# Optimization experiments

Hardware: AMD Instinct MI355X
Metric: run time of the kernel (lower is better)

The kernel has to match this reference:

```python
import jax, jax.numpy as jnp
import numpy as np

N = 100_000          # nodes
E_RAND = 1_600_000   # random edges (avg degree 16)
IN, H, F, SEQ = 64, 4, 16, 10
FLAT = H * F * SEQ   # 640, MLP input width
MLP_DIMS = [FLAT, 180, 150, 128, 80, 64, 32, 1]


def setup_inputs() -> dict:
    key = jax.random.key(0)
    ks = jax.random.split(key, 32)
    x = jax.random.normal(ks[0], (N, IN), jnp.float32)
    # edges + self loops (dgl.add_self_loop)
    src = jnp.concatenate([jax.random.randint(ks[1], (E_RAND,), 0, N), jnp.arange(N)]).astype(jnp.int32)
    dst = jnp.concatenate([jax.random.randint(ks[2], (E_RAND,), 0, N), jnp.arange(N)]).astype(jnp.int32)
    inp = {"x": x, "src": src, "dst": dst}
    # GATConv params (fc has no bias in DGL; bias added post-aggregation)
    inp["fc_w"] = (jax.random.normal(ks[3], (IN, H * F), jnp.float32) / np.sqrt(IN).astype(np.float32))
    inp["bias"] = jnp.zeros((H * F,), jnp.float32)
    inp["attn_l"] = jax.random.normal(ks[4], (H, F), jnp.float32) * 0.1
    inp["attn_r"] = jax.random.normal(ks[5], (H, F), jnp.float32) * 0.1
    # deep MLP params
    for i in range(7):
        di, do = MLP_DIMS[i], MLP_DIMS[i + 1]
        inp[f"w{i+1}"] = jax.random.normal(ks[6 + i], (di, do), jnp.float32) / np.sqrt(di).astype(np.float32)
        inp[f"b{i+1}"] = jnp.zeros((do,), jnp.float32)
    inp["wt"] = jax.random.normal(ks[20], (FLAT, 1), jnp.float32) / np.sqrt(FLAT).astype(np.float32)
    return inp


def reference(x, src, dst, fc_w, bias, attn_l, attn_r,
              w1, b1, w2, b2, w3, b3, w4, b4, w5, b5, w6, b6, w7, b7, wt):
    # --- GATConv ---
    feat = (x @ fc_w).reshape(N, H, F)                      # [N,H,F]
    el = jnp.einsum('nhf,hf->nh', feat, attn_l)             # [N,H]
    er = jnp.einsum('nhf,hf->nh', feat, attn_r)
    e = jax.nn.leaky_relu(el[src] + er[dst], 0.2)           # [E,H]
    # edge softmax over incoming edges of each dst node
    m = jax.ops.segment_max(e, dst, num_segments=N)         # [N,H]
    ez = jnp.exp(e - m[dst])
    denom = jax.ops.segment_sum(ez, dst, num_segments=N)
    alpha = ez / denom[dst]                                 # [E,H]
    msg = alpha[:, :, None] * feat[src]                     # [E,H,F]
    out = jax.ops.segment_sum(msg, dst, num_segments=N) + bias.reshape(1, H, F)
    # --- flatten SEQ nodes per path, deep MLP + linear_trans ---
    g = out.reshape(N // SEQ, FLAT)                         # [P,640]
    h = g
    layers = [(w1, b1), (w2, b2), (w3, b3), (w4, b4), (w5, b5), (w6, b6), (w7, b7)]
    for i, (w, b) in enumerate(layers):
        h = h @ w + b
        if i < len(layers) - 1:
            h = jax.nn.relu(h)
    wx = g @ wt                                             # [P,1]
    return h + wx
```

## Files before the change

kernel.cpp:

```cpp
#include <hip/hip_runtime.h>
#include <hip/hip_bf16.h>
#include <hip/hip_fp16.h>

#define N_NODES 100000
#define P_PATHS 10000
#define NBUK 391
#define FEAT_BLKS 782
#define HIST_BLKS 416
#define WPREP_BLKS 94
#define LOG2E 1.4426950408889634f
#define BC_CAP 5120

typedef __attribute__((ext_vector_type(8))) short s16x8;
typedef __attribute__((ext_vector_type(4))) short s16x4;
typedef __attribute__((ext_vector_type(4))) float f32x4;
typedef __attribute__((ext_vector_type(8))) _Float16 f16x8;
typedef __attribute__((ext_vector_type(2))) _Float16 f16x2;

__device__ __forceinline__ short f2bf(float v) {
    return __builtin_bit_cast(short, __float2bfloat16(v));
}
__device__ __forceinline__ float bf2f(short s) {
    return __bfloat162float(__builtin_bit_cast(__hip_bfloat16, s));
}
__device__ __forceinline__ float h2f(short s) {
    return __half2float(__builtin_bit_cast(__half, s));
}
__device__ __forceinline__ short f2h(float v) {
    return __builtin_bit_cast(short, __float2half(v));
}

__global__ __launch_bounds__(256) void k_fused1(const float* __restrict__ x,
                                                const float* __restrict__ fc_w,
                                                const float* __restrict__ attn_l,
                                                const float* __restrict__ attn_r,
                                                __half* __restrict__ feat,
                                                float* __restrict__ el,
                                                float* __restrict__ er,
                                                const int* __restrict__ dst,
                                                int* __restrict__ buktot,
                                                const float* __restrict__ w1,
                                                const float* __restrict__ w2,
                                                const float* __restrict__ w3,
                                                const float* __restrict__ w4,
                                                const float* __restrict__ w5,
                                                const float* __restrict__ w6,
                                                short* __restrict__ wf, int E) {
    __shared__ float s_w[64 * 64];
    __shared__ float s_wx[64 * 16];
    __shared__ int hcnt[NBUK];
    int tid = threadIdx.x;
    int bb = blockIdx.x;

    if (bb < FEAT_BLKS) {
        for (int i = tid; i < 4096; i += 256) s_w[i] = fc_w[i];
        __syncthreads();
        for (int i = tid; i < 1024; i += 256) {
            int k = i >> 4, c = i & 15;
            float v = 0.f;
            if (c < 8) {
                int h = c & 3;
                const float* av = (c < 4) ? attn_l : attn_r;
                for (int f = 0; f < 16; ++f) v += s_w[k * 64 + h * 16 + f] * av[h * 16 + f];
            }
            s_wx[i] = v * LOG2E;
        }
        __syncthreads();

        int w = tid >> 6, l = tid & 63;
        int c_lane = l & 15, kg = l >> 4;

        s16x8 wh[5][2], wlo[5][2];
#pragma unroll
        for (int ct = 0; ct < 5; ++ct)
#pragma unroll
            for (int ks = 0; ks < 2; ++ks) {
                s16x8 h8, l8;
#pragma unroll
                for (int i = 0; i < 8; ++i) {
                    int k = ks * 32 + kg * 8 + i;
                    float v = (ct < 4) ? s_w[k * 64 + ct * 16 + c_lane]
                                       : s_wx[k * 16 + c_lane];
                    short hi = f2bf(v);
                    h8[i] = hi;
                    l8[i] = f2bf(v - bf2f(hi));
                }
                wh[ct][ks] = h8;
                wlo[ct][ks] = l8;
            }

        int nbase = bb * 128 + w * 32;
#pragma unroll 1
        for (int mt = 0; mt < 2; ++mt) {
            int m0 = nbase + mt * 16;
            if (m0 >= N_NODES) break;
            int arow = m0 + c_lane;
            size_t axoff = (size_t)(arow < N_NODES ? arow : N_NODES - 1) * 64;
            s16x8 ah[2], alo[2];
#pragma unroll
            for (int ks = 0; ks < 2; ++ks) {
                const float* xp = x + axoff + ks * 32 + kg * 8;
                float4 v0 = *(const float4*)xp;
                float4 v1 = *(const float4*)(xp + 4);
                float vv[8] = {v0.x, v0.y, v0.z, v0.w, v1.x, v1.y, v1.z, v1.w};
                s16x8 h8, l8;
#pragma unroll
                for (int i = 0; i < 8; ++i) {
                    short hi = f2bf(vv[i]);
                    h8[i] = hi;
                    l8[i] = f2bf(vv[i] - bf2f(hi));
                }
                ah[ks] = h8;
                alo[ks] = l8;
            }
            int r0 = m0 + kg * 4;
#pragma unroll
            for (int ct = 0; ct < 5; ++ct) {
                f32x4 acc = {0.f, 0.f, 0.f, 0.f};
#pragma unroll
                for (int ks = 0; ks < 2; ++ks) {
                    acc = __builtin_amdgcn_mfma_f32_16x16x32_bf16(ah[ks], wh[ct][ks], acc, 0, 0, 0);
                    acc = __builtin_amdgcn_mfma_f32_16x16x32_bf16(ah[ks], wlo[ct][ks], acc, 0, 0, 0);
                    acc = __builtin_amdgcn_mfma_f32_16x16x32_bf16(alo[ks], wh[ct][ks], acc, 0, 0, 0);
                }
                if (ct < 4) {
#pragma unroll
                    for (int j = 0; j < 4; ++j) {
                        int r = r0 + j;
                        if (r < N_NODES)
                            feat[(size_t)r * 64 + ct * 16 + c_lane] = __float2half(acc[j]);
                    }
                } else {
                    if (c_lane < 4) {
#pragma unroll
                        for (int j = 0; j < 4; ++j) {
                            int r = r0 + j;
                            if (r < N_NODES) el[r * 4 + c_lane] = acc[j];
                        }
                    } else if (c_lane < 8) {
#pragma unroll
                        for (int j = 0; j < 4; ++j) {
                            int r = r0 + j;
                            if (r < N_NODES) er[r * 4 + (c_lane - 4)] = acc[j];
                        }
                    }
                }
            }
        }
    } else if (bb < FEAT_BLKS + HIST_BLKS) {
        int hb = bb - FEAT_BLKS;
        for (int i = tid; i < NBUK; i += 256) hcnt[i] = 0;
        __syncthreads();
#pragma unroll
        for (int j = 0; j < 4; ++j) {
            int i = hb * 4096 + j * 1024 + tid * 4;
            if (i + 3 < E) {
                int4 d4 = *(const int4*)(dst + i);
                atomicAdd(&hcnt[d4.x >> 8], 1);
                atomicAdd(&hcnt[d4.y >> 8], 1);
                atomicAdd(&hcnt[d4.z >> 8], 1);
                atomicAdd(&hcnt[d4.w >> 8], 1);
            } else {
                for (int k = i; k < E && k < i + 4; ++k)
                    atomicAdd(&hcnt[dst[k] >> 8], 1);
            }
        }
        __syncthreads();
        for (int i = tid; i < NBUK; i += 256)
            if (hcnt[i]) atomicAdd(buktot + i, hcnt[i]);
    } else {
        const int nblk[6] = {240, 60, 40, 20, 12, 4};
        const int din_[6] = {640, 180, 150, 128, 80, 64};
        const int dout_[6] = {180, 150, 128, 80, 64, 32};
        const int ks_[6]  = {20, 6, 5, 4, 3, 2};
        const int off_[6] = {0, 122880, 153600, 174080, 184320, 190464};
        const float* wp[6] = {w1, w2, w3, w4, w5, w6};

        int b = (bb - FEAT_BLKS - HIST_BLKS) * 4 + (tid >> 6);
        int layer = 0;
        while (layer < 5 && b >= nblk[layer]) { b -= nblk[layer]; ++layer; }
        int KS = ks_[layer];
        int ct = b / KS, ks = b % KS;
        int l = tid & 63;
        int c = ct * 16 + (l & 15);
        int k0 = ks * 32 + ((l >> 4) * 8);
        int din = din_[layer], dout = dout_[layer];
        const float* w = wp[layer];
        s16x8 vh;
#pragma unroll
        for (int i = 0; i < 8; ++i) {
            int k = k0 + i;
            float v = (k < din && c < dout) ? w[k * dout + c] : 0.f;
            vh[i] = f2h(v);
        }
        size_t o = (size_t)off_[layer] + ((size_t)(ct * KS + ks) * 64 + l) * 8;
        *(s16x8*)(wf + o) = vh;
    }
}

__global__ __launch_bounds__(512) void k_scanB(const int* __restrict__ buktot,
                                               int* __restrict__ bukstart,
                                               int* __restrict__ bukptr,
                                               int* __restrict__ rowptr, int E) {
    __shared__ int s[512];
    int tid = threadIdx.x;
    int v = (tid < NBUK) ? buktot[tid] : 0;
    s[tid] = v;
    __syncthreads();
    for (int off = 1; off < 512; off <<= 1) {
        int t = (tid >= off) ? s[tid - off] : 0;
        __syncthreads();
        s[tid] += t;
        __syncthreads();
    }
    int excl = s[tid] - v;
    if (tid < NBUK) { bukstart[tid] = excl; bukptr[tid] = excl; }
    if (tid == 0) { bukstart[NBUK] = E; rowptr[N_NODES] = E; }
}

__global__ __launch_bounds__(256) void k_bucketA(const int* __restrict__ src,
                                                 const int* __restrict__ dst,
                                                 int* __restrict__ bukptr,
                                                 unsigned* __restrict__ pair, int E) {
    __shared__ int cnt[NBUK];
    __shared__ int seg[NBUK];
    __shared__ int gbase[NBUK];
    __shared__ unsigned sbuf[2048];
    __shared__ int gaddr[2048];
    __shared__ int csum[256];
    int tid = threadIdx.x;
    for (int i = tid; i < NBUK; i += 256) cnt[i] = 0;
    __syncthreads();
    int b0 = blockIdx.x * 2048;
    int sv[8], dv[8], off[8];
#pragma unroll
    for (int j = 0; j < 8; ++j) {
        int i = b0 + j * 256 + tid;
        if (i < E) {
            sv[j] = src[i];
            dv[j] = dst[i];
            off[j] = atomicAdd(&cnt[dv[j] >> 8], 1);
        } else {
            dv[j] = -1; sv[j] = 0; off[j] = 0;
        }
    }
    __syncthreads();
    int c0 = (2 * tid < NBUK) ? cnt[2 * tid] : 0;
    int c1 = (2 * tid + 1 < NBUK) ? cnt[2 * tid + 1] : 0;
    int psum = c0 + c1;
    csum[tid] = psum;
    __syncthreads();
    for (int o2 = 1; o2 < 256; o2 <<= 1) {
        int t = (tid >= o2) ? csum[tid - o2] : 0;
        __syncthreads();
        csum[tid] += t;
        __syncthreads();
    }
    int pexcl = csum[tid] - psum;
    if (2 * tid < NBUK) seg[2 * tid] = pexcl;
    if (2 * tid + 1 < NBUK) seg[2 * tid + 1] = pexcl + c0;
    __syncthreads();
    for (int i = tid; i < NBUK; i += 256)
        gbase[i] = cnt[i] ? atomicAdd(bukptr + i, cnt[i]) : 0;
    __syncthreads();
#pragma unroll
    for (int j = 0; j < 8; ++j) {
        if (dv[j] >= 0) {
            int b = dv[j] >> 8;
            int k = seg[b] + off[j];
            sbuf[k] = (unsigned)sv[j] | ((unsigned)(dv[j] & 255) << 17);
            gaddr[k] = gbase[b] + off[j];
        }
    }
    __syncthreads();
    int tot = E - b0; if (tot > 2048) tot = 2048;
    for (int k = tid; k < tot; k += 256)
        pair[gaddr[k]] = sbuf[k];
}

__global__ __launch_bounds__(256) void k_bucketC(const unsigned* __restrict__ pair,
                                                 const int* __restrict__ bukstart,
                                                 int* __restrict__ rowptr,
                                                 int* __restrict__ csr, int E) {
    __shared__ int cnt[256];
    __shared__ int s[256];
    __shared__ int wofs[256];
    __shared__ unsigned sp[BC_CAP];
    int buk = blockIdx.x, tid = threadIdx.x;
    int p0 = bukstart[buk], p1 = bukstart[buk + 1];
    int len = p1 - p0;
    bool fits = (len <= BC_CAP);
    cnt[tid] = 0;
    __syncthreads();
    for (int i = p0 + tid; i < p1; i += 256) {
        unsigned v = pair[i];
        if (fits) sp[i - p0] = v;
        atomicAdd(&cnt[v >> 17], 1);
    }
    __syncthreads();
    int v = cnt[tid];
    s[tid] = v;
    __syncthreads();
    for (int off = 1; off < 256; off <<= 1) {
        int t = (tid >= off) ? s[tid - off] : 0;
        __syncthreads();
        s[tid] += t;
        __syncthreads();
    }
    int r = p0 + s[tid] - v;
    wofs[tid] = r;
    int node = (buk << 8) + tid;
    if (node < N_NODES) rowptr[node] = r;
    __syncthreads();
    for (int i = p0 + tid; i < p1; i += 256) {
        unsigned p = fits ? sp[i - p0] : pair[i];
        int pos = atomicAdd(&wofs[p >> 17], 1);
        csr[pos] = (int)(p & 0x1FFFFu);
    }
}

__global__ __launch_bounds__(256) void k_agg(const int* __restrict__ rowptr,
                                             const int* __restrict__ csr,
                                             const float* __restrict__ el,
                                             const float* __restrict__ er,
                                             const __half* __restrict__ feat,
                                             const float* __restrict__ bias,
                                             __half* __restrict__ agg) {
    int tid = threadIdx.x;
    int wave = tid >> 6, lane = tid & 63;
    int slot = lane >> 3;
    int fl = lane & 7;
    int bid = blockIdx.x;
    int swz = (bid & 7) * 3125 + (bid >> 3);
    int n = swz * 4 + wave;
    if (n >= N_NODES) return;
    int h = fl >> 1;
    float ern = er[(size_t)n * 4 + h];
    int e0 = rowptr[n], e1 = rowptr[n + 1];
    float acc[8] = {0.f, 0.f, 0.f, 0.f, 0.f, 0.f, 0.f, 0.f};
    float den = 0.f;
    const f16x2 one2 = {(_Float16)1.f, (_Float16)1.f};
    int e = e0 + slot;
    for (; e + 8 < e1; e += 16) {
        int s0 = csr[e], s1 = csr[e + 8];
        f16x8 v0 = *(const f16x8*)(feat + (size_t)s0 * 64 + fl * 8);
        f16x8 v1 = *(const f16x8*)(feat + (size_t)s1 * 64 + fl * 8);
        float ev0 = el[(size_t)s0 * 4 + h] + ern;
        float ev1 = el[(size_t)s1 * 4 + h] + ern;
        ev0 = ev0 > 0.f ? ev0 : 0.2f * ev0;
        ev1 = ev1 > 0.f ? ev1 : 0.2f * ev1;
        float ez0 = __builtin_amdgcn_exp2f(ev0);
        float ez1 = __builtin_amdgcn_exp2f(ev1);
        f16x2 ezp = {(_Float16)ez0, (_Float16)ez1};
#pragma unroll
        for (int t = 0; t < 8; ++t) {
            f16x2 p = {v0[t], v1[t]};
            acc[t] = __builtin_amdgcn_fdot2(p, ezp, acc[t], false);
        }
        den = __builtin_amdgcn_fdot2(one2, ezp, den, false);
    }
    for (; e < e1; e += 8) {
        int s0 = csr[e];
        f16x8 v0 = *(const f16x8*)(feat + (size_t)s0 * 64 + fl * 8);
        float ev0 = el[(size_t)s0 * 4 + h] + ern;
        ev0 = ev0 > 0.f ? ev0 : 0.2f * ev0;
        float ez0 = __builtin_amdgcn_exp2f(ev0);
#pragma unroll
        for (int t = 0; t < 8; ++t)
            acc[t] += ez0 * (float)v0[t];
        den += ez0;
    }
#pragma unroll
    for (int t = 0; t < 8; ++t) {
        acc[t] += __shfl_xor(acc[t], 32);
        acc[t] += __shfl_xor(acc[t], 16);
        acc[t] += __shfl_xor(acc[t], 8);
    }
    den += __shfl_xor(den, 32);
    den += __shfl_xor(den, 16);
    den += __shfl_xor(den, 8);
    if (slot == 0) {
        float inv = 1.f / den;
        s16x8 o;
#pragma unroll
        for (int t = 0; t < 8; ++t)
            o[t] = f2h(acc[t] * inv + bias[fl * 8 + t]);
        *(s16x8*)(agg + (size_t)n * 64 + fl * 8) = o;
    }
}

template <int KS, int CT>
__device__ __forceinline__ void mfma_layer16(const short* sa, int sstride,
                                             short* dst_,
                                             const short* __restrict__ wf,
                                             const float* __restrict__ bias,
                                             int dout, int w, int l) {
    int abase = (l & 15) * sstride + ((l >> 4) * 8);
    int c_lane = l & 15;
    for (int ct = w; ct < CT; ct += 4) {
        f32x4 acc = {0.f, 0.f, 0.f, 0.f};
        const f16x8* wp = (const f16x8*)wf + (size_t)(ct * KS) * 64 + l;
#pragma unroll
        for (int ks = 0; ks < KS; ++ks) {
            f16x8 av = *(const f16x8*)(sa + abase + ks * 32);
            f16x8 wv = wp[ks * 64];
            acc = __builtin_amdgcn_mfma_f32_16x16x32_f16(av, wv, acc, 0, 0, 0);
        }
        int c = ct * 16 + c_lane;
        float bb = (c < dout) ? bias[c] : 0.f;
        int row0 = (l >> 4) * 4;
#pragma unroll
        for (int j = 0; j < 4; ++j) {
            float v = acc[j] + bb;
            v = v > 0.f ? v : 0.f;
            dst_[(row0 + j) * 200 + c] = f2h(v);
        }
    }
}

__global__ __launch_bounds__(256) void k_mlp(const __half* __restrict__ agg,
                                             const short* __restrict__ wf,
                                             const float* __restrict__ b1,
                                             const float* __restrict__ b2,
                                             const float* __restrict__ b3,
                                             const float* __restrict__ b4,
                                             const float* __restrict__ b5,
                                             const float* __restrict__ b6,
                                             const float* __restrict__ w7,
                                             const float* __restrict__ b7,
                                             const float* __restrict__ wt,
                                             float* __restrict__ outp) {
    __shared__ __align__(16) short smem[13600];
    __shared__ float wx[16];
    short* g  = smem;
    short* h0 = smem + 10368;
    short* h1 = smem;

    int tid = threadIdx.x;
    int w = tid >> 6, l = tid & 63;
    int p0 = blockIdx.x * 16;

    const s16x8* a8 = (const s16x8*)(agg + (size_t)p0 * 640);
    for (int i = tid; i < 16 * 80; i += 256) {
        int r = i / 80, c8 = (i % 80) * 8;
        *(s16x8*)(g + r * 648 + c8) = a8[i];
    }

    if (tid < 128) {
        int path = tid >> 3, sub = tid & 7;
        const __half* gr = agg + (size_t)(p0 + path) * 640;
        float acc = 0.f;
        for (int k = sub * 4; k < 640; k += 32) {
            s16x4 gv = *(const s16x4*)(gr + k);
            float4 wv = *(const float4*)(wt + k);
            acc += h2f(gv[0]) * wv.x + h2f(gv[1]) * wv.y
                 + h2f(gv[2]) * wv.z + h2f(gv[3]) * wv.w;
        }
        acc += __shfl_xor(acc, 1);
        acc += __shfl_xor(acc, 2);
        acc += __shfl_xor(acc, 4);
        if (sub == 0) wx[path] = acc;
    }
    __syncthreads();

    mfma_layer16<20, 12>(g, 648, h0, wf + 0,      b1, 180, w, l);
    __syncthreads();
    mfma_layer16<6, 10>(h0, 200, h1, wf + 122880, b2, 150, w, l);
    __syncthreads();
    mfma_layer16<5, 8>(h1, 200, h0, wf + 153600, b3, 128, w, l);
    __syncthreads();
    mfma_layer16<4, 5>(h0, 200, h1, wf + 174080, b4, 80, w, l);
    {
        int r = tid >> 4, c = 80 + (tid & 15);
        h1[r * 200 + c] = 0;
    }
    __syncthreads();
    mfma_layer16<3, 4>(h1, 200, h0, wf + 184320, b5, 64, w, l);
    __syncthreads();
    mfma_layer16<2, 2>(h0, 200, h1, wf + 190464, b6, 32, w, l);
    __syncthreads();

    if (tid < 16) {
        float acc = b7[0];
#pragma unroll
        for (int k = 0; k < 32; ++k)
            acc += h2f(h1[tid * 200 + k]) * w7[k];
        outp[p0 + tid] = acc + wx[tid];
    }
}

extern "C" void kernel_launch(void* const* d_in, const int* in_sizes, int n_in,
                              void* d_out, int out_size, void* d_ws, size_t ws_size,
                              hipStream_t stream) {
    const float* x      = (const float*)d_in[0];
    const int*   src    = (const int*)d_in[1];
    const int*   dst    = (const int*)d_in[2];
    const float* fc_w   = (const float*)d_in[3];
    const float* bias   = (const float*)d_in[4];
    const float* attn_l = (const float*)d_in[5];
    const float* attn_r = (const float*)d_in[6];
    const float* w1 = (const float*)d_in[7];  const float* b1 = (const float*)d_in[8];
    const float* w2 = (const float*)d_in[9];  const float* b2 = (const float*)d_in[10];
    const float* w3 = (const float*)d_in[11]; const float* b3 = (const float*)d_in[12];
    const float* w4 = (const float*)d_in[13]; const float* b4 = (const float*)d_in[14];
    const float* w5 = (const float*)d_in[15]; const float* b5 = (const float*)d_in[16];
    const float* w6 = (const float*)d_in[17]; const float* b6 = (const float*)d_in[18];
    const float* w7 = (const float*)d_in[19]; const float* b7 = (const float*)d_in[20];
    const float* wt = (const float*)d_in[21];
    int E = in_sizes[1];

    float* ws      = (float*)d_ws;
    __half* feat   = (__half*)ws;
    float* el      = ws + 6400000;
    float* er      = ws + 6800000;
    __half* agg    = (__half*)(ws + 7200000);
    unsigned* pair = (unsigned*)(ws + 10400000);
    int*   rowptr  = (int*)(ws + 13600000);
    int*   buktot  = (int*)(ws + 13700004);
    int*   bukstart= (int*)(ws + 13700400);
    int*   bukptr  = (int*)(ws + 13700800);
    int*   csr     = (int*)(ws + 13701200);
    short* wf      = (short*)(ws + 13701200 + E);

    int nwgA = (E + 2047) / 2048;

    hipMemsetAsync(buktot, 0, NBUK * 4, stream);

    k_fused1<<<FEAT_BLKS + HIST_BLKS + WPREP_BLKS, 256, 0, stream>>>(
        x, fc_w, attn_l, attn_r, feat, el, er, dst, buktot,
        w1, w2, w3, w4, w5, w6, wf, E);
    k_scanB<<<1, 512, 0, stream>>>(buktot, bukstart, bukptr, rowptr, E);
    k_bucketA<<<nwgA, 256, 0, stream>>>(src, dst, bukptr, pair, E);
    k_bucketC<<<NBUK, 256, 0, stream>>>(pair, bukstart, rowptr, csr, E);
    k_agg<<<N_NODES / 4, 256, 0, stream>>>(rowptr, csr, el, er, feat, bias, agg);
    k_mlp<<<P_PATHS / 16, 256, 0, stream>>>(agg, wf, b1, b2, b3, b4, b5, b6,
                                            w7, b7, wt, (float*)d_out);
}
```

Baseline: 154.5 us.

## Fold bucket scan into bucketA and use single fp16 MFMA for feature projection

Removes the single-block k_scanB kernel: every bucketA block now recomputes the exclusive scan of bucket totals itself and takes its global base from a second zeroed counter array plus that scan. Block 0 also writes bukstart and rowptr. Separately, the feature projection GEMM drops the 3-term bf16 split (hi/lo) in favour of one fp16 MFMA per k-step, cutting MFMA count and conversion work at some cost in precision. This saves a kernel launch and its serialization gap in exchange for redundant scan work in every block.

```diff
diff --git a/kernel.cpp b/kernel.cpp
--- a/kernel.cpp
+++ b/kernel.cpp
@@ -17,12 +17,6 @@
 typedef __attribute__((ext_vector_type(8))) _Float16 f16x8;
 typedef __attribute__((ext_vector_type(2))) _Float16 f16x2;
 
-__device__ __forceinline__ short f2bf(float v) {
-    return __builtin_bit_cast(short, __float2bfloat16(v));
-}
-__device__ __forceinline__ float bf2f(short s) {
-    return __bfloat162float(__builtin_bit_cast(__hip_bfloat16, s));
-}
 __device__ __forceinline__ float h2f(short s) {
     return __half2float(__builtin_bit_cast(__half, s));
 }
@@ -70,23 +64,20 @@
         int w = tid >> 6, l = tid & 63;
         int c_lane = l & 15, kg = l >> 4;
 
-        s16x8 wh[5][2], wlo[5][2];
+        f16x8 wfr[5][2];
 #pragma unroll
         for (int ct = 0; ct < 5; ++ct)
 #pragma unroll
             for (int ks = 0; ks < 2; ++ks) {
-                s16x8 h8, l8;
+                f16x8 h8;
 #pragma unroll
                 for (int i = 0; i < 8; ++i) {
                     int k = ks * 32 + kg * 8 + i;
                     float v = (ct < 4) ? s_w[k * 64 + ct * 16 + c_lane]
                                        : s_wx[k * 16 + c_lane];
-                    short hi = f2bf(v);
-                    h8[i] = hi;
-                    l8[i] = f2bf(v - bf2f(hi));
+                    h8[i] = (_Float16)v;
                 }
-                wh[ct][ks] = h8;
-                wlo[ct][ks] = l8;
+                wfr[ct][ks] = h8;
             }
 
         int nbase = bb * 128 + w * 32;
@@ -96,33 +87,26 @@
             if (m0 >= N_NODES) break;
             int arow = m0 + c_lane;
             size_t axoff = (size_t)(arow < N_NODES ? arow : N_NODES - 1) * 64;
-            s16x8 ah[2], alo[2];
+            f16x8 af[2];
 #pragma unroll
             for (int ks = 0; ks < 2; ++ks) {
                 const float* xp = x + axoff + ks * 32 + kg * 8;
                 float4 v0 = *(const float4*)xp;
                 float4 v1 = *(const float4*)(xp + 4);
-                float vv[8] = {v0.x, v0.y, v0.z, v0.w, v1.x, v1.y, v1.z, v1.w};
-                s16x8 h8, l8;
-#pragma unroll
-                for (int i = 0; i < 8; ++i) {
-                    short hi = f2bf(vv[i]);
-                    h8[i] = hi;
-                    l8[i] = f2bf(vv[i] - bf2f(hi));
-                }
-                ah[ks] = h8;
-                alo[ks] = l8;
+                f16x8 h8;
+                h8[0] = (_Float16)v0.x; h8[1] = (_Float16)v0.y;
+                h8[2] = (_Float16)v0.z; h8[3] = (_Float16)v0.w;
+                h8[4] = (_Float16)v1.x; h8[5] = (_Float16)v1.y;
+                h8[6] = (_Float16)v1.z; h8[7] = (_Float16)v1.w;
+                af[ks] = h8;
             }
             int r0 = m0 + kg * 4;
 #pragma unroll
             for (int ct = 0; ct < 5; ++ct) {
                 f32x4 acc = {0.f, 0.f, 0.f, 0.f};
 #pragma unroll
-                for (int ks = 0; ks < 2; ++ks) {
-                    acc = __builtin_amdgcn_mfma_f32_16x16x32_bf16(ah[ks], wh[ct][ks], acc, 0, 0, 0);
-                    acc = __builtin_amdgcn_mfma_f32_16x16x32_bf16(ah[ks], wlo[ct][ks], acc, 0, 0, 0);
-                    acc = __builtin_amdgcn_mfma_f32_16x16x32_bf16(alo[ks], wh[ct][ks], acc, 0, 0, 0);
-                }
+                for (int ks = 0; ks < 2; ++ks)
+                    acc = __builtin_amdgcn_mfma_f32_16x16x32_f16(af[ks], wfr[ct][ks], acc, 0, 0, 0);
                 if (ct < 4) {
 #pragma unroll
                     for (int j = 0; j < 4; ++j) {
@@ -198,37 +182,42 @@
     }
 }
 
-__global__ __launch_bounds__(512) void k_scanB(const int* __restrict__ buktot,
-                                               int* __restrict__ bukstart,
-                                               int* __restrict__ bukptr,
-                                               int* __restrict__ rowptr, int E) {
-    __shared__ int s[512];
-    int tid = threadIdx.x;
-    int v = (tid < NBUK) ? buktot[tid] : 0;
-    s[tid] = v;
-    __syncthreads();
-    for (int off = 1; off < 512; off <<= 1) {
-        int t = (tid >= off) ? s[tid - off] : 0;
-        __syncthreads();
-        s[tid] += t;
-        __syncthreads();
-    }
-    int excl = s[tid] - v;
-    if (tid < NBUK) { bukstart[tid] = excl; bukptr[tid] = excl; }
-    if (tid == 0) { bukstart[NBUK] = E; rowptr[N_NODES] = E; }
-}
-
 __global__ __launch_bounds__(256) void k_bucketA(const int* __restrict__ src,
                                                  const int* __restrict__ dst,
-                                                 int* __restrict__ bukptr,
+                                                 const int* __restrict__ buktot,
+                                                 int* __restrict__ bukcnt2,
+                                                 int* __restrict__ bukstart,
+                                                 int* __restrict__ rowptr,
                                                  unsigned* __restrict__ pair, int E) {
     __shared__ int cnt[NBUK];
+    __shared__ int gexc[NBUK];
     __shared__ int seg[NBUK];
     __shared__ int gbase[NBUK];
     __shared__ unsigned sbuf[2048];
     __shared__ int gaddr[2048];
     __shared__ int csum[256];
     int tid = threadIdx.x;
+
+    int g0 = (2 * tid < NBUK) ? buktot[2 * tid] : 0;
+    int g1 = (2 * tid + 1 < NBUK) ? buktot[2 * tid + 1] : 0;
+    int gsum = g0 + g1;
+    csum[tid] = gsum;
+    __syncthreads();
+    for (int o2 = 1; o2 < 256; o2 <<= 1) {
+        int t = (tid >= o2) ? csum[tid - o2] : 0;
+        __syncthreads();
+        csum[tid] += t;
+        __syncthreads();
+    }
+    int gex = csum[tid] - gsum;
+    if (2 * tid < NBUK) gexc[2 * tid] = gex;
+    if (2 * tid + 1 < NBUK) gexc[2 * tid + 1] = gex + g0;
+    __syncthreads();
+    if (blockIdx.x == 0) {
+        for (int i = tid; i < NBUK; i += 256) bukstart[i] = gexc[i];
+        if (tid == 0) { bukstart[NBUK] = E; rowptr[N_NODES] = E; }
+    }
+
     for (int i = tid; i < NBUK; i += 256) cnt[i] = 0;
     __syncthreads();
     int b0 = blockIdx.x * 2048;
@@ -261,7 +250,7 @@
     if (2 * tid + 1 < NBUK) seg[2 * tid + 1] = pexcl + c0;
     __syncthreads();
     for (int i = tid; i < NBUK; i += 256)
-        gbase[i] = cnt[i] ? atomicAdd(bukptr + i, cnt[i]) : 0;
+        gbase[i] = cnt[i] ? (gexc[i] + atomicAdd(bukcnt2 + i, cnt[i])) : 0;
     __syncthreads();
 #pragma unroll
     for (int j = 0; j < 8; ++j) {
@@ -517,20 +506,20 @@
     unsigned* pair = (unsigned*)(ws + 10400000);
     int*   rowptr  = (int*)(ws + 13600000);
     int*   buktot  = (int*)(ws + 13700004);
-    int*   bukstart= (int*)(ws + 13700400);
-    int*   bukptr  = (int*)(ws + 13700800);
+    int*   bukcnt2 = (int*)(ws + 13700395);
+    int*   bukstart= (int*)(ws + 13700800);
     int*   csr     = (int*)(ws + 13701200);
     short* wf      = (short*)(ws + 13701200 + E);
 
     int nwgA = (E + 2047) / 2048;
 
-    hipMemsetAsync(buktot, 0, NBUK * 4, stream);
+    hipMemsetAsync(buktot, 0, 2 * NBUK * 4, stream);
 
     k_fused1<<<FEAT_BLKS + HIST_BLKS + WPREP_BLKS, 256, 0, stream>>>(
         x, fc_w, attn_l, attn_r, feat, el, er, dst, buktot,
         w1, w2, w3, w4, w5, w6, wf, E);
-    k_scanB<<<1, 512, 0, stream>>>(buktot, bukstart, bukptr, rowptr, E);
-    k_bucketA<<<nwgA, 256, 0, stream>>>(src, dst, bukptr, pair, E);
+    k_bucketA<<<nwgA, 256, 0, stream>>>(src, dst, buktot, bukcnt2, bukstart,
+                                        rowptr, pair, E);
     k_bucketC<<<NBUK, 256, 0, stream>>>(pair, bukstart, rowptr, csr, E);
     k_agg<<<N_NODES / 4, 256, 0, stream>>>(rowptr, csr, el, er, feat, bias, agg);
     k_mlp<<<P_PATHS / 16, 256, 0, stream>>>(agg, wf, b1, b2, b3, b4, b5, b6,
```

After: 166.1 us. 7.5% more time.
